# Optimization experiments

Measured on AMD Instinct MI355X. Metric: run time of the kernel, lower is better.

## Reference

```python
import jax, jax.numpy as jnp
import numpy as np
from jax import lax

BN_EPS = 1e-5

# Straight-through-estimator sign (XNOR-Net BinActive): fwd=sign, bwd=clipped identity
@jax.custom_vjp
def ste_sign(x):
    return jnp.sign(x)

def _ste_fwd(x):
    return jnp.sign(x), x

def _ste_bwd(x, g):
    return (g * (jnp.abs(x) <= 1.0).astype(g.dtype),)

ste_sign.defvjp(_ste_fwd, _ste_bwd)

def conv2d(x, w):
    # x: NCHW, w: OIHW, stride 1, VALID
    return lax.conv_general_dilated(x, w, (1, 1), 'VALID',
                                    dimension_numbers=('NCHW', 'OIHW', 'NCHW'))

def maxpool2(x):
    return lax.reduce_window(x, -jnp.inf, lax.max, (1, 1, 2, 2), (1, 1, 2, 2), 'VALID')

def bn2d(x, gamma, beta):
    # training-mode BatchNorm2d: batch stats over (N,H,W), biased variance
    mean = jnp.mean(x, axis=(0, 2, 3), keepdims=True)
    var = jnp.mean((x - mean) ** 2, axis=(0, 2, 3), keepdims=True)
    xhat = (x - mean) * lax.rsqrt(var + BN_EPS)
    return xhat * gamma[None, :, None, None] + beta[None, :, None, None]

def bn1d(x, gamma, beta):
    mean = jnp.mean(x, axis=0, keepdims=True)
    var = jnp.mean((x - mean) ** 2, axis=0, keepdims=True)
    xhat = (x - mean) * lax.rsqrt(var + BN_EPS)
    return xhat * gamma[None, :] + beta[None, :]

def bin_conv2d(x, w):
    # XNOR-style: binarize input and weight, scale by per-filter alpha = mean|W|
    alpha = jnp.mean(jnp.abs(w), axis=(1, 2, 3))  # [O]
    out = conv2d(ste_sign(x), ste_sign(w))
    return out * alpha[None, :, None, None]

def bin_linear(x, w):
    # w: [out_features, in_features]
    alpha = jnp.mean(jnp.abs(w), axis=1)  # [out_features]
    return (ste_sign(x) @ ste_sign(w).T) * alpha[None, :]


def setup_inputs() -> dict:
    key = jax.random.key(0)
    ks = jax.random.split(key, 8)
    B = 8192
    inp = {
        'x': jax.random.normal(ks[0], (B, 1, 28, 28), dtype=jnp.float32),
        'conv1_w': jax.random.normal(ks[1], (20, 1, 5, 5), dtype=jnp.float32) * 0.2,
        'bn1_g': jnp.ones((20,), jnp.float32),
        'bn1_b': jnp.zeros((20,), jnp.float32),
        'conv2_w': jax.random.normal(ks[2], (50, 20, 5, 5), dtype=jnp.float32) * 0.04,
        'bn2_g': jnp.ones((50,), jnp.float32),
        'bn2_b': jnp.zeros((50,), jnp.float32),
        'fc1_w': jax.random.normal(ks[3], (500, 800), dtype=jnp.float32) * 0.035,
        'bn3_g': jnp.ones((500,), jnp.float32),
        'bn3_b': jnp.zeros((500,), jnp.float32),
        'fc2_w': jax.random.normal(ks[4], (10, 500), dtype=jnp.float32) * 0.045,
        'fc2_b': jnp.zeros((10,), jnp.float32),
    }
    return inp


def reference(x, conv1_w, bn1_g, bn1_b, conv2_w, bn2_g, bn2_b,
              fc1_w, bn3_g, bn3_b, fc2_w, fc2_b):
    h = conv2d(x, conv1_w)                 # [B,20,24,24]
    h = jax.nn.relu(bn2d(h, bn1_g, bn1_b))
    h = maxpool2(h)                        # [B,20,12,12]
    h = bin_conv2d(h, conv2_w)             # [B,50,8,8]
    h = jax.nn.relu(bn2d(h, bn2_g, bn2_b))
    h = maxpool2(h)                        # [B,50,4,4]
    h = h.reshape(-1, 50 * 4 * 4)          # [B,800]
    h = bin_linear(h, fc1_w)               # [B,500]
    h = jax.nn.relu(bn1d(h, bn3_g, bn3_b))
    return h @ fc2_w.T + fc2_b[None, :]    # [B,10]
```

## Files before the change

kernel.cpp:

```cpp
#include <hip/hip_runtime.h>
#include <stdint.h>

#define BATCH 8192
#define NJOB  1179648

__global__ __launch_bounds__(256) void k_pack(const float* __restrict__ w2,
    const float* __restrict__ w3, unsigned* __restrict__ wpos2,
    unsigned* __restrict__ wneg2, float* __restrict__ alpha2,
    unsigned* __restrict__ wpos3, unsigned* __restrict__ wneg3,
    float* __restrict__ alpha3, int* __restrict__ flags2, int* __restrict__ flags3){
  __shared__ int zf;
  int tid = threadIdx.x;
  if (tid == 0) zf = 0;
  __syncthreads();
  if (blockIdx.x < 5){
    int t = blockIdx.x*256 + tid;
    int had0 = 0;
    if (t < 1250){
      int o = t/25, k = t%25;
      unsigned p=0, n=0;
      for (int i=0;i<20;i++){
        float v = w2[(o*20+i)*25 + k];
        if (v > 0.f) p |= 1u<<i;
        else if (v < 0.f) n |= 1u<<i;
        else had0 = 1;
      }
      wpos2[t] = p; wneg2[t] = n;
    }
    if (t < 50){
      float s = 0.f;
      for (int i=0;i<500;i++) s += fabsf(w2[t*500+i]);
      alpha2[t] = s / 500.f;
    }
    if (had0) atomicOr(&zf, 1);
    __syncthreads();
    if (tid == 0) flags2[blockIdx.x] = zf;
  } else {
    int t = (blockIdx.x-5)*256 + tid;
    int had0 = 0;
    if (t < 12500){
      int j = t/25, w = t%25;
      unsigned p=0, n=0;
      for (int bb=0;bb<32;bb++){
        float v = w3[j*800 + w*32 + bb];
        if (v > 0.f) p |= 1u<<bb;
        else if (v < 0.f) n |= 1u<<bb;
        else had0 = 1;
      }
      wpos3[t] = p; wneg3[t] = n;
    }
    if (t < 500){
      float s = 0.f;
      for (int i=0;i<800;i++) s += fabsf(w3[t*800+i]);
      alpha3[t] = s / 800.f;
    }
    if (had0) atomicOr(&zf, 1);
    __syncthreads();
    if (tid == 0) flags3[blockIdx.x-5] = zf;
  }
}


#define CONV1_ROWS(IPTR)                                                      \
  float vA0=0.f,vA1=0.f,vA2=0.f,vA3=0.f;                                      \
  float vB0=0.f,vB1=0.f,vB2=0.f,vB3=0.f;                                      \
  _Pragma("unroll")                                                           \
  for (int r=0;r<6;r++){                                                      \
    const float2* rp = (const float2*)((IPTR) + r*28);                        \
    float2 p0 = rp[0], p1 = rp[1], p2 = rp[2];                                \
    float row0=p0.x, row1=p0.y, row2=p1.x, row3=p1.y, row4=p2.x, row5=p2.y;   \
    if (r<5){                                                                 \
      _Pragma("unroll")                                                       \
      for (int kx=0;kx<5;kx++){                                               \
        float e0 = (kx==0?row0:kx==1?row1:kx==2?row2:kx==3?row3:row4);        \
        float e1 = (kx==0?row1:kx==1?row2:kx==2?row3:kx==3?row4:row5);        \
        float w = wa[r*5+kx], u = wb[r*5+kx];                                 \
        vA0=fmaf(e0,w,vA0); vA1=fmaf(e1,w,vA1);                               \
        vB0=fmaf(e0,u,vB0); vB1=fmaf(e1,u,vB1);                               \
      }                                                                       \
    }                                                                         \
    if (r>0){                                                                 \
      _Pragma("unroll")                                                       \
      for (int kx=0;kx<5;kx++){                                               \
        float e0 = (kx==0?row0:kx==1?row1:kx==2?row2:kx==3?row3:row4);        \
        float e1 = (kx==0?row1:kx==1?row2:kx==2?row3:kx==3?row4:row5);        \
        float w = wa[(r-1)*5+kx], u = wb[(r-1)*5+kx];                         \
        vA2=fmaf(e0,w,vA2); vA3=fmaf(e1,w,vA3);                               \
        vB2=fmaf(e0,u,vB2); vB3=fmaf(e1,u,vB3);                               \
      }                                                                       \
    }                                                                         \
  }

template<bool STORE_MM>
__global__ __launch_bounds__(256) void k_conv1_stats(const float* __restrict__ x,
        const float* __restrict__ w1, const float* __restrict__ g1,
        float* __restrict__ part1, float2* __restrict__ c1ext){
  __shared__ float img[8*784];
  __shared__ float wsh[500];
  __shared__ float gsh[20];
  __shared__ float red[4][40];
  int tid = threadIdx.x;
  size_t base = (size_t)blockIdx.x * 8;
  const float4* xv = (const float4*)(x + base*784);
  float4* iv = (float4*)img;
  for (int i=tid;i<1568;i+=256) iv[i] = xv[i];
  for (int i=tid;i<500;i+=256)  wsh[i] = w1[i];
  if (tid < 20) gsh[tid] = g1[tid];
  __syncthreads();
  int lane = tid & 63, wid = tid >> 6;
#pragma unroll 1
  for (int cg=0; cg<10; ++cg){
    float wa[25], wb[25];
#pragma unroll
    for (int k=0;k<25;k++){ wa[k]=wsh[(2*cg)*25+k]; wb[k]=wsh[(2*cg+1)*25+k]; }
    float gA = gsh[2*cg], gB = gsh[2*cg+1];
    float sa=0.f, qa=0.f, sb=0.f, qb=0.f;
#pragma unroll 1
    for (int job=tid; job<8*144; job+=256){
      int li = job/144, pp = job%144;
      int py = pp/12, px = pp%12;
      const float* ip = &img[li*784 + py*56 + px*2];
      CONV1_ROWS(ip)
      sa += (vA0+vA1)+(vA2+vA3);
      qa = fmaf(vA0,vA0, fmaf(vA1,vA1, fmaf(vA2,vA2, fmaf(vA3,vA3, qa))));
      sb += (vB0+vB1)+(vB2+vB3);
      qb = fmaf(vB0,vB0, fmaf(vB1,vB1, fmaf(vB2,vB2, fmaf(vB3,vB3, qb))));
      if (STORE_MM){
        float mxA = fmaxf(fmaxf(vA0,vA1),fmaxf(vA2,vA3));
        float mnA = fminf(fminf(vA0,vA1),fminf(vA2,vA3));
        float mxB = fmaxf(fmaxf(vB0,vB1),fmaxf(vB2,vB3));
        float mnB = fminf(fminf(vB0,vB1),fminf(vB2,vB3));
        float eA = (gA > 0.f) ? mxA : mnA;
        float eB = (gB > 0.f) ? mxB : mnB;
        c1ext[(size_t)cg*NJOB + (base+li)*144 + pp] = make_float2(eA,eB);
      }
    }
#pragma unroll
    for (int d=32; d>0; d>>=1){
      sa += __shfl_down(sa,d); qa += __shfl_down(qa,d);
      sb += __shfl_down(sb,d); qb += __shfl_down(qb,d);
    }
    if (lane==0){
      red[wid][(2*cg)*2]   = sa; red[wid][(2*cg)*2+1]   = qa;
      red[wid][(2*cg+1)*2] = sb; red[wid][(2*cg+1)*2+1] = qb;
    }
  }
  __syncthreads();
  if (tid < 40)
    part1[blockIdx.x*40 + tid] = red[0][tid]+red[1][tid]+red[2][tid]+red[3][tid];
}

__global__ __launch_bounds__(256) void k_reduce1(const float* __restrict__ part1,
        const float* __restrict__ g, const float* __restrict__ b,
        float* __restrict__ s1t1){
  __shared__ double rs[256], rq[256];
  int c = blockIdx.x;
  int tid = threadIdx.x;
  double s=0.0, q=0.0;
  for (int i=tid;i<1024;i+=256){
    s += (double)part1[i*40 + c*2];
    q += (double)part1[i*40 + c*2 + 1];
  }
  rs[tid]=s; rq[tid]=q;
  __syncthreads();
  for (int d=128; d>0; d>>=1){
    if (tid<d){ rs[tid]+=rs[tid+d]; rq[tid]+=rq[tid+d]; }
    __syncthreads();
  }
  if (tid==0){
    double N = 8192.0*576.0;
    double mean = rs[0]/N, var = rq[0]/N - mean*mean;
    double r = 1.0/sqrt(var + 1e-5);
    double sc = (double)g[c]*r;
    s1t1[c*2]   = (float)sc;
    s1t1[c*2+1] = (float)((double)b[c] - mean*sc);
  }
}

__global__ __launch_bounds__(256) void k_conv1_bin(const float* __restrict__ x,
        const float* __restrict__ w1, const float* __restrict__ s1t1,
        unsigned* __restrict__ mask1){
  __shared__ float img[8*784];
  __shared__ float wsh[500];
  __shared__ float st[40];
  __shared__ unsigned lw[8*144];
  int tid = threadIdx.x;
  size_t base = (size_t)blockIdx.x * 8;
  const float4* xv = (const float4*)(x + base*784);
  float4* iv = (float4*)img;
  for (int i=tid;i<1568;i+=256) iv[i] = xv[i];
  for (int i=tid;i<500;i+=256)  wsh[i] = w1[i];
  for (int i=tid;i<8*144;i+=256) lw[i] = 0u;
  if (tid < 40) st[tid] = s1t1[tid];
  __syncthreads();
#pragma unroll 1
  for (int cg=0; cg<10; ++cg){
    float wa[25], wb[25];
#pragma unroll
    for (int k=0;k<25;k++){ wa[k]=wsh[(2*cg)*25+k]; wb[k]=wsh[(2*cg+1)*25+k]; }
    float sA = st[(2*cg)*2],   tA = st[(2*cg)*2+1];
    float sB = st[(2*cg+1)*2], tB = st[(2*cg+1)*2+1];
#pragma unroll 1
    for (int job=tid; job<8*144; job+=256){
      int li = job/144, pp = job%144;
      int py = pp/12, px = pp%12;
      const float* ip = &img[li*784 + py*56 + px*2];
      CONV1_ROWS(ip)
      unsigned bA = (fmaf(vA0,sA,tA) > 0.f) || (fmaf(vA1,sA,tA) > 0.f) ||
                    (fmaf(vA2,sA,tA) > 0.f) || (fmaf(vA3,sA,tA) > 0.f);
      unsigned bB = (fmaf(vB0,sB,tB) > 0.f) || (fmaf(vB1,sB,tB) > 0.f) ||
                    (fmaf(vB2,sB,tB) > 0.f) || (fmaf(vB3,sB,tB) > 0.f);
      lw[job] |= (bA << (2*cg)) | (bB << (2*cg+1));
    }
  }
  __syncthreads();
  for (int i=tid;i<8*144;i+=256){
    int li = i/144, pp = i%144;
    mask1[(base+li)*144 + pp] = lw[i];
  }
}

__global__ __launch_bounds__(256) void k_conv1_bin_lite(const float2* __restrict__ c1ext,
        const float* __restrict__ s1t1, unsigned* __restrict__ mask1){
  __shared__ float st[40];
  int tid = threadIdx.x;
  if (tid < 40) st[tid] = s1t1[tid];
  __syncthreads();
  int J = blockIdx.x*256 + tid;
  unsigned word = 0;
#pragma unroll
  for (int cg=0; cg<10; ++cg){
    float2 v = c1ext[(size_t)cg*NJOB + J];
    float sA = st[4*cg+0], tA = st[4*cg+1];
    float sB = st[4*cg+2], tB = st[4*cg+3];
    word |= ((fmaf(v.x,sA,tA) > 0.f) ? 1u : 0u) << (2*cg);
    word |= ((fmaf(v.y,sB,tB) > 0.f) ? 1u : 0u) << (2*cg+1);
  }
  mask1[J] = word;
}

__global__ __launch_bounds__(256) void k_conv2(const unsigned* __restrict__ mask1,
    const unsigned* __restrict__ wpos, const unsigned* __restrict__ wneg,
    const int* __restrict__ flags2, short* __restrict__ S16){
  __shared__ unsigned m1[4*144];
  __shared__ __align__(16) unsigned wp[1400], wn[1400];
  int tid = threadIdx.x;
  size_t base = (size_t)blockIdx.x * 4;
  bool slow = (flags2[0]|flags2[1]|flags2[2]|flags2[3]|flags2[4]) != 0;
  for (int i=tid;i<4*144;i+=256) m1[i] = mask1[base*144 + i];
  for (int i=tid;i<1400;i+=256){
    int o = i/28, k = i%28;
    wn[i] = (k<25) ? wneg[o*25+k] : 0u;
    if (slow) wp[i] = (k<25) ? wpos[o*25+k] : 0u;
  }
  __syncthreads();
  int lane = tid & 63, wid = tid >> 6;
  int y2 = lane >> 3, x2 = lane & 7;
  unsigned mw[25];
  const unsigned* mrow = &m1[wid*144];
#pragma unroll
  for (int ky=0;ky<5;ky++)
#pragma unroll
    for (int kx=0;kx<5;kx++)
      mw[ky*5+kx] = mrow[(y2+ky)*12 + x2+kx];
  short* sp = &S16[((base+wid)*50)*64 + lane];
  if (!slow){
    int pbase = 0;
#pragma unroll
    for (int k=0;k<25;k++) pbase += __popc(mw[k]);
#pragma unroll 1
    for (int o=0;o<50;o++){
      const uint4* n4 = (const uint4*)&wn[o*28];
      int Sn=0;
#pragma unroll
      for (int g=0; g<6; g++){
        uint4 N = n4[g];
        Sn += __popc(mw[4*g]&N.x) + __popc(mw[4*g+1]&N.y)
            + __popc(mw[4*g+2]&N.z) + __popc(mw[4*g+3]&N.w);
      }
      Sn += __popc(mw[24] & wn[o*28+24]);
      sp[o*64] = (short)(pbase - 2*Sn);
    }
  } else {
#pragma unroll 1
    for (int o=0;o<50;o++){
      const uint4* p4 = (const uint4*)&wp[o*28];
      const uint4* n4 = (const uint4*)&wn[o*28];
      int Sp=0, Sn=0;
#pragma unroll
      for (int g=0; g<6; g++){
        uint4 P = p4[g], N = n4[g];
        Sp += __popc(mw[4*g]&P.x) + __popc(mw[4*g+1]&P.y)
            + __popc(mw[4*g+2]&P.z) + __popc(mw[4*g+3]&P.w);
        Sn += __popc(mw[4*g]&N.x) + __popc(mw[4*g+1]&N.y)
            + __popc(mw[4*g+2]&N.z) + __popc(mw[4*g+3]&N.w);
      }
      Sp += __popc(mw[24] & wp[o*28+24]);
      Sn += __popc(mw[24] & wn[o*28+24]);
      sp[o*64] = (short)(Sp - Sn);
    }
  }
}

__global__ __launch_bounds__(256) void k_stats2(const short* __restrict__ S16,
        int* __restrict__ part2){
  int tid = threadIdx.x;
  int lane = tid & 63, wid = tid >> 6;
  const short* p = S16 + (size_t)blockIdx.x * 32 * 3200;
  int rs[13], rq[13];
#pragma unroll
  for (int k=0;k<13;k++){ rs[k]=0; rq[k]=0; }
#pragma unroll 1
  for (int im=0; im<32; ++im){
    const short* q = p + im*3200 + tid;
#pragma unroll
    for (int k=0;k<13;k++){
      if (wid + 4*k < 50){
        int v = q[256*k];
        rs[k] += v; rq[k] += v*v;
      }
    }
  }
#pragma unroll
  for (int k=0;k<13;k++){
    int o = wid + 4*k;
    if (o < 50){
      int s = rs[k], q2 = rq[k];
#pragma unroll
      for (int d=32; d>0; d>>=1){ s += __shfl_down(s,d); q2 += __shfl_down(q2,d); }
      if (lane==0){
        part2[blockIdx.x*100 + o*2]     = s;
        part2[blockIdx.x*100 + o*2 + 1] = q2;
      }
    }
  }
}

__global__ __launch_bounds__(256) void k_conv2_stats_legacy(const unsigned* __restrict__ mask1,
    const unsigned* __restrict__ wpos, const unsigned* __restrict__ wneg,
    const int* __restrict__ flags2, int* __restrict__ part2){
  __shared__ unsigned m1[4*144];
  __shared__ __align__(16) unsigned wp[1400], wn[1400];
  __shared__ int red[4][100];
  int tid = threadIdx.x;
  size_t base = (size_t)blockIdx.x * 4;
  bool slow = (flags2[0]|flags2[1]|flags2[2]|flags2[3]|flags2[4]) != 0;
  for (int i=tid;i<4*144;i+=256) m1[i] = mask1[base*144 + i];
  for (int i=tid;i<1400;i+=256){
    int o = i/28, k = i%28;
    wn[i] = (k<25) ? wneg[o*25+k] : 0u;
    wp[i] = (k<25) ? wpos[o*25+k] : 0u;
  }
  __syncthreads();
  int lane = tid & 63, wid = tid >> 6;
  int y2 = lane >> 3, x2 = lane & 7;
  unsigned mw[25];
  const unsigned* mrow = &m1[wid*144];
#pragma unroll
  for (int ky=0;ky<5;ky++)
#pragma unroll
    for (int kx=0;kx<5;kx++)
      mw[ky*5+kx] = mrow[(y2+ky)*12 + x2+kx];
#pragma unroll 1
  for (int o=0;o<50;o++){
    const uint4* p4 = (const uint4*)&wp[o*28];
    const uint4* n4 = (const uint4*)&wn[o*28];
    int Sp=0, Sn=0;
#pragma unroll
    for (int g=0; g<6; g++){
      uint4 P = p4[g], N = n4[g];
      Sp += __popc(mw[4*g]&P.x) + __popc(mw[4*g+1]&P.y)
          + __popc(mw[4*g+2]&P.z) + __popc(mw[4*g+3]&P.w);
      Sn += __popc(mw[4*g]&N.x) + __popc(mw[4*g+1]&N.y)
          + __popc(mw[4*g+2]&N.z) + __popc(mw[4*g+3]&N.w);
    }
    Sp += __popc(mw[24] & wp[o*28+24]);
    Sn += __popc(mw[24] & wn[o*28+24]);
    int S = Sp - Sn;
    int rs = S, rq = S*S;
#pragma unroll
    for (int d=32; d>0; d>>=1){ rs += __shfl_down(rs,d); rq += __shfl_down(rq,d); }
    if (lane==0){ red[wid][o*2] = rs; red[wid][o*2+1] = rq; }
  }
  __syncthreads();
  if (tid < 100)
    part2[blockIdx.x*100 + tid] = red[0][tid]+red[1][tid]+red[2][tid]+red[3][tid];
}

__global__ __launch_bounds__(256) void k_reduce2(const int* __restrict__ part2,
        int nchunk, const float* __restrict__ alpha2, const float* __restrict__ g,
        const float* __restrict__ b, float* __restrict__ s2t2){
  __shared__ long long rs[256], rq[256];
  int o = blockIdx.x;
  int tid = threadIdx.x;
  long long s=0, q=0;
  for (int i=tid;i<nchunk;i+=256){
    s += part2[i*100 + o*2];
    q += part2[i*100 + o*2 + 1];
  }
  rs[tid]=s; rq[tid]=q;
  __syncthreads();
  for (int d=128; d>0; d>>=1){
    if (tid<d){ rs[tid]+=rs[tid+d]; rq[tid]+=rq[tid+d]; }
    __syncthreads();
  }
  if (tid==0){
    double N = 8192.0*64.0;
    double meanS = (double)rs[0]/N, E2 = (double)rq[0]/N;
    double varS = E2 - meanS*meanS;
    double a = (double)alpha2[o];
    double mean_g = a*meanS, var_g = a*a*varS;
    double r = 1.0/sqrt(var_g + 1e-5);
    double sc = (double)g[o]*r;
    s2t2[o*2]   = (float)(sc*a);
    s2t2[o*2+1] = (float)((double)b[o] - mean_g*sc);
  }
}

#define BIN2_POOL_BODY                                                        \
    unsigned long long bal = __ballot(cond);                                  \
    unsigned long long t4 = bal | (bal>>1) | (bal>>8) | (bal>>9);             \
    bool pb = (lane < 16) && ((t4 >> (16*(lane>>2) + 2*(lane&3))) & 1ull);    \
    unsigned long long bal2 = __ballot(pb);                                   \
    if (lane==0){                                                             \
      unsigned pooled16 = (unsigned)(bal2 & 0xFFFFull);                       \
      lw[wid*25 + (o>>1)] |= pooled16 << (16*(o&1));                          \
    }

__global__ __launch_bounds__(256) void k_bin2(const unsigned* __restrict__ mask1,
    const unsigned* __restrict__ wpos, const unsigned* __restrict__ wneg,
    const float* __restrict__ s2t2, unsigned* __restrict__ mask2){
  __shared__ unsigned m1[4*144];
  __shared__ __align__(16) unsigned wp[1400], wn[1400];
  __shared__ float st[100];
  __shared__ unsigned lw[100];
  int tid = threadIdx.x;
  size_t base = (size_t)blockIdx.x * 4;
  for (int i=tid;i<4*144;i+=256) m1[i] = mask1[base*144 + i];
  for (int i=tid;i<1400;i+=256){
    int o = i/28, k = i%28;
    wp[i] = (k<25) ? wpos[o*25+k] : 0u;
    wn[i] = (k<25) ? wneg[o*25+k] : 0u;
  }
  if (tid < 100){ st[tid] = s2t2[tid]; lw[tid] = 0u; }
  __syncthreads();
  int lane = tid & 63, wid = tid >> 6;
  int y2 = lane >> 3, x2 = lane & 7;
  unsigned mw[25];
  const unsigned* mrow = &m1[wid*144];
#pragma unroll
  for (int ky=0;ky<5;ky++)
#pragma unroll
    for (int kx=0;kx<5;kx++)
      mw[ky*5+kx] = mrow[(y2+ky)*12 + x2+kx];
#pragma unroll 1
  for (int o=0;o<50;o++){
    const uint4* p4 = (const uint4*)&wp[o*28];
    const uint4* n4 = (const uint4*)&wn[o*28];
    int Sp=0, Sn=0;
#pragma unroll
    for (int g=0; g<6; g++){
      uint4 P = p4[g], N = n4[g];
      Sp += __popc(mw[4*g]&P.x) + __popc(mw[4*g+1]&P.y)
          + __popc(mw[4*g+2]&P.z) + __popc(mw[4*g+3]&P.w);
      Sn += __popc(mw[4*g]&N.x) + __popc(mw[4*g+1]&N.y)
          + __popc(mw[4*g+2]&N.z) + __popc(mw[4*g+3]&N.w);
    }
    Sp += __popc(mw[24] & wp[o*28+24]);
    Sn += __popc(mw[24] & wn[o*28+24]);
    int S = Sp - Sn;
    bool cond = fmaf((float)S, st[o*2], st[o*2+1]) > 0.f;
    BIN2_POOL_BODY
  }
  __syncthreads();
  if (tid < 100) mask2[base*25 + tid] = lw[tid];
}

__global__ __launch_bounds__(256) void k_bin2_lite(const short* __restrict__ S16,
    const float* __restrict__ s2t2, unsigned* __restrict__ mask2){
  __shared__ float st[100];
  __shared__ unsigned lw[100];
  int tid = threadIdx.x;
  if (tid < 100){ st[tid] = s2t2[tid]; lw[tid] = 0u; }
  __syncthreads();
  int lane = tid & 63, wid = tid >> 6;
  size_t img = (size_t)blockIdx.x*4 + wid;
#pragma unroll 1
  for (int o=0;o<50;o++){
    int S = S16[(img*50 + o)*64 + lane];
    bool cond = fmaf((float)S, st[o*2], st[o*2+1]) > 0.f;
    BIN2_POOL_BODY
  }
  __syncthreads();
  if (tid < 100) mask2[blockIdx.x*100 + tid] = lw[tid];
}

__global__ __launch_bounds__(256) void k_fc1(const unsigned* __restrict__ mask2,
    const unsigned* __restrict__ wpos, const unsigned* __restrict__ wneg,
    const int* __restrict__ flags3, short* __restrict__ S3){
  __shared__ unsigned m2s[8*25];
  __shared__ short s3s[8*500];
  int tid = threadIdx.x;
  size_t base = (size_t)blockIdx.x * 8;
  for (int i=tid;i<200;i+=256) m2s[i] = mask2[base*25 + i];
  __syncthreads();
  int f = 0;
  for (int i=0;i<49;i++) f |= flags3[i];
  int bl = tid & 7;
  int jg = tid >> 3;
  const unsigned* mrow = &m2s[bl*25];
  if (f == 0){
    int pbase = 0;
#pragma unroll
    for (int w=0;w<25;w++) pbase += __popc(mrow[w]);
#pragma unroll 1
    for (int j=jg; j<500; j+=32){
      const unsigned* n = &wneg[j*25];
      int Sn = 0;
#pragma unroll
      for (int w=0;w<25;w++) Sn += __popc(mrow[w] & n[w]);
      s3s[bl*500 + j] = (short)(pbase - 2*Sn);
    }
  } else {
#pragma unroll 1
    for (int j=jg; j<500; j+=32){
      const unsigned* p = &wpos[j*25];
      const unsigned* n = &wneg[j*25];
      int S = 0;
#pragma unroll
      for (int w=0;w<25;w++){
        unsigned m = mrow[w];
        S += __popc(m & p[w]) - __popc(m & n[w]);
      }
      s3s[bl*500 + j] = (short)S;
    }
  }
  __syncthreads();
  for (int i=tid;i<8*500;i+=256) S3[base*500 + i] = s3s[i];
}

__global__ __launch_bounds__(256) void k_stats3(const short* __restrict__ S3,
                                                int* __restrict__ part3){
  int tid = threadIdx.x;
  const short* p = &S3[(size_t)blockIdx.x * 64 * 500];
  int s0=0,q0=0,s1=0,q1=0;
  for (int b=0;b<64;b++){
    int v0 = p[b*500 + tid];
    s0 += v0; q0 += v0*v0;
    if (tid < 244){
      int v1 = p[b*500 + tid + 256];
      s1 += v1; q1 += v1*v1;
    }
  }
  part3[blockIdx.x*1000 + tid*2]     = s0;
  part3[blockIdx.x*1000 + tid*2 + 1] = q0;
  if (tid < 244){
    part3[blockIdx.x*1000 + (tid+256)*2]     = s1;
    part3[blockIdx.x*1000 + (tid+256)*2 + 1] = q1;
  }
}

__global__ void k_reduce3(const int* __restrict__ part3, const float* __restrict__ alpha3,
                          const float* __restrict__ g, const float* __restrict__ b,
                          float* __restrict__ s3t3){
  int j = blockIdx.x*256 + threadIdx.x;
  if (j >= 500) return;
  long long s=0, q=0;
  for (int i=0;i<128;i++){
    s += part3[i*1000 + j*2];
    q += part3[i*1000 + j*2 + 1];
  }
  double N = 8192.0;
  double meanS = (double)s/N, E2 = (double)q/N;
  double varS = E2 - meanS*meanS;
  double a = (double)alpha3[j];
  double mean_u = a*meanS, var_u = a*a*varS;
  double r = 1.0/sqrt(var_u + 1e-5);
  double sc = (double)g[j]*r;
  s3t3[j*2]   = (float)(sc*a);
  s3t3[j*2+1] = (float)((double)b[j] - mean_u*sc);
}

__global__ __launch_bounds__(256) void k_final(const short* __restrict__ S3,
    const float* __restrict__ s3t3, const float* __restrict__ fc2w,
    const float* __restrict__ fc2b, float* __restrict__ out){
  __shared__ float w[5000];
  __shared__ float st[1000];
  __shared__ float bias[10];
  int tid = threadIdx.x;
  for (int i=tid;i<5000;i+=256) w[i] = fc2w[i];
  for (int i=tid;i<1000;i+=256) st[i] = s3t3[i];
  if (tid<10) bias[tid] = fc2b[tid];
  __syncthreads();
  int sub = tid & 7;
  int li  = tid >> 3;
  size_t b = (size_t)blockIdx.x*32 + li;
  const short* sp = &S3[b*500];
  float acc[10];
#pragma unroll
  for (int m=0;m<10;m++) acc[m] = 0.f;
#pragma unroll 1
  for (int j=sub; j<500; j+=8){
    float h = fmaf((float)sp[j], st[j*2], st[j*2+1]);
    h = fmaxf(h, 0.f);
#pragma unroll
    for (int m=0;m<10;m++) acc[m] = fmaf(h, w[m*500+j], acc[m]);
  }
#pragma unroll
  for (int m=0;m<10;m++){
    float v = acc[m];
    v += __shfl_xor(v, 1);
    v += __shfl_xor(v, 2);
    v += __shfl_xor(v, 4);
    acc[m] = v;
  }
  if (sub == 0){
#pragma unroll
    for (int m=0;m<10;m++) out[b*10 + m] = acc[m] + bias[m];
  }
}

extern "C" void kernel_launch(void* const* d_in, const int* in_sizes, int n_in,
                              void* d_out, int out_size, void* d_ws, size_t ws_size,
                              hipStream_t stream){
  const float* x    = (const float*)d_in[0];
  const float* w1   = (const float*)d_in[1];
  const float* bn1g = (const float*)d_in[2];
  const float* bn1b = (const float*)d_in[3];
  const float* w2   = (const float*)d_in[4];
  const float* bn2g = (const float*)d_in[5];
  const float* bn2b = (const float*)d_in[6];
  const float* w3   = (const float*)d_in[7];
  const float* bn3g = (const float*)d_in[8];
  const float* bn3b = (const float*)d_in[9];
  const float* w4   = (const float*)d_in[10];
  const float* b4   = (const float*)d_in[11];
  float* out = (float*)d_out;
  (void)in_sizes; (void)n_in; (void)out_size;

  char* wsb = (char*)d_ws;
  size_t off = 0;
  auto alloc = [&](size_t n){ size_t o = off; off = (off + n + 255) & ~(size_t)255; return o; };
  float*    s1t1   = (float*)(wsb + alloc(40*sizeof(float)));
  float*    s2t2   = (float*)(wsb + alloc(100*sizeof(float)));
  float*    s3t3   = (float*)(wsb + alloc(1000*sizeof(float)));
  float*    alpha2 = (float*)(wsb + alloc(50*sizeof(float)));
  float*    alpha3 = (float*)(wsb + alloc(500*sizeof(float)));
  int*      flags2 = (int*)(wsb + alloc(5*4));
  int*      flags3 = (int*)(wsb + alloc(49*4));
  unsigned* wpos2  = (unsigned*)(wsb + alloc(1250*4));
  unsigned* wneg2  = (unsigned*)(wsb + alloc(1250*4));
  unsigned* wpos3  = (unsigned*)(wsb + alloc(12500*4));
  unsigned* wneg3  = (unsigned*)(wsb + alloc(12500*4));
  float*    part1  = (float*)(wsb + alloc(1024*40*4));
  int*      part2  = (int*)(wsb + alloc(2048*100*4));
  int*      part3  = (int*)(wsb + alloc(128*1000*4));
  unsigned* mask1  = (unsigned*)(wsb + alloc((size_t)BATCH*144*4));
  unsigned* mask2  = (unsigned*)(wsb + alloc((size_t)BATCH*25*4));
  short*    S3     = (short*)(wsb + alloc((size_t)BATCH*500*2));
  short*    S16    = (short*)(wsb + alloc((size_t)BATCH*50*64*2));
  bool useS16 = (ws_size >= off);
  float2*   c1ext  = (float2*)(wsb + alloc((size_t)10*NJOB*8));
  bool useMM  = (ws_size >= off);

  hipLaunchKernelGGL(k_pack, dim3(54), dim3(256), 0, stream,
                     w2, w3, wpos2, wneg2, alpha2, wpos3, wneg3, alpha3, flags2, flags3);
  if (useMM)
    hipLaunchKernelGGL(HIP_KERNEL_NAME(k_conv1_stats<true>),  dim3(1024), dim3(256), 0, stream, x, w1, bn1g, part1, c1ext);
  else
    hipLaunchKernelGGL(HIP_KERNEL_NAME(k_conv1_stats<false>), dim3(1024), dim3(256), 0, stream, x, w1, bn1g, part1, c1ext);
  hipLaunchKernelGGL(k_reduce1,      dim3(20),    dim3(256), 0, stream, part1, bn1g, bn1b, s1t1);
  if (useMM)
    hipLaunchKernelGGL(k_conv1_bin_lite, dim3(4608), dim3(256), 0, stream, c1ext, s1t1, mask1);
  else
    hipLaunchKernelGGL(k_conv1_bin,  dim3(1024),  dim3(256), 0, stream, x, w1, s1t1, mask1);
  if (useS16){
    hipLaunchKernelGGL(k_conv2,      dim3(2048),  dim3(256), 0, stream, mask1, wpos2, wneg2, flags2, S16);
    hipLaunchKernelGGL(k_stats2,     dim3(256),   dim3(256), 0, stream, S16, part2);
    hipLaunchKernelGGL(k_reduce2,    dim3(50),    dim3(256), 0, stream, part2, 256, alpha2, bn2g, bn2b, s2t2);
    hipLaunchKernelGGL(k_bin2_lite,  dim3(2048),  dim3(256), 0, stream, S16, s2t2, mask2);
  } else {
    hipLaunchKernelGGL(k_conv2_stats_legacy, dim3(2048), dim3(256), 0, stream, mask1, wpos2, wneg2, flags2, part2);
    hipLaunchKernelGGL(k_reduce2,    dim3(50),    dim3(256), 0, stream, part2, 2048, alpha2, bn2g, bn2b, s2t2);
    hipLaunchKernelGGL(k_bin2,       dim3(2048),  dim3(256), 0, stream, mask1, wpos2, wneg2, s2t2, mask2);
  }
  hipLaunchKernelGGL(k_fc1,          dim3(1024),  dim3(256), 0, stream, mask2, wpos3, wneg3, flags3, S3);
  hipLaunchKernelGGL(k_stats3,       dim3(128),   dim3(256), 0, stream, S3, part3);
  hipLaunchKernelGGL(k_reduce3,      dim3(2),     dim3(256), 0, stream, part3, alpha3, bn3g, bn3b, s3t3);
  hipLaunchKernelGGL(k_final,        dim3(256),   dim3(256), 0, stream, S3, s3t3, w4, b4, out);
}
```

Before: 327.3 us.

## Fuse conv1 binarization into conv2 and BN2-pool into fc1 with stats

```diff
diff --git a/kernel.cpp b/kernel.cpp
--- a/kernel.cpp
+++ b/kernel.cpp
@@ -220,23 +220,81 @@
   }
 }
 
-__global__ __launch_bounds__(256) void k_conv1_bin_lite(const float2* __restrict__ c1ext,
-        const float* __restrict__ s1t1, unsigned* __restrict__ mask1){
+__global__ __launch_bounds__(256) void k_conv2f(const float2* __restrict__ c1ext,
+    const float* __restrict__ s1t1, const unsigned* __restrict__ wpos,
+    const unsigned* __restrict__ wneg, const int* __restrict__ flags2,
+    short* __restrict__ S16){
+  __shared__ unsigned m1[4*144];
   __shared__ float st[40];
-  int tid = threadIdx.x;
+  __shared__ __align__(16) unsigned wp[1400], wn[1400];
+  int tid = threadIdx.x;
+  size_t base = (size_t)blockIdx.x * 4;
+  bool slow = (flags2[0]|flags2[1]|flags2[2]|flags2[3]|flags2[4]) != 0;
   if (tid < 40) st[tid] = s1t1[tid];
-  __syncthreads();
-  int J = blockIdx.x*256 + tid;
-  unsigned word = 0;
-#pragma unroll
-  for (int cg=0; cg<10; ++cg){
-    float2 v = c1ext[(size_t)cg*NJOB + J];
-    float sA = st[4*cg+0], tA = st[4*cg+1];
-    float sB = st[4*cg+2], tB = st[4*cg+3];
-    word |= ((fmaf(v.x,sA,tA) > 0.f) ? 1u : 0u) << (2*cg);
-    word |= ((fmaf(v.y,sB,tB) > 0.f) ? 1u : 0u) << (2*cg+1);
-  }
-  mask1[J] = word;
+  for (int i=tid;i<1400;i+=256){
+    int o = i/28, k = i%28;
+    wn[i] = (k<25) ? wneg[o*25+k] : 0u;
+    if (slow) wp[i] = (k<25) ? wpos[o*25+k] : 0u;
+  }
+  __syncthreads();
+  for (int job=tid; job<4*144; job+=256){
+    int li = job/144, pp = job%144;
+    unsigned word = 0;
+#pragma unroll
+    for (int cg=0; cg<10; ++cg){
+      float2 v = c1ext[(size_t)cg*NJOB + (base+li)*144 + pp];
+      word |= ((fmaf(v.x, st[4*cg+0], st[4*cg+1]) > 0.f) ? 1u : 0u) << (2*cg);
+      word |= ((fmaf(v.y, st[4*cg+2], st[4*cg+3]) > 0.f) ? 1u : 0u) << (2*cg+1);
+    }
+    m1[job] = word;
+  }
+  __syncthreads();
+  int lane = tid & 63, wid = tid >> 6;
+  int y2 = lane >> 3, x2 = lane & 7;
+  unsigned mw[25];
+  const unsigned* mrow = &m1[wid*144];
+#pragma unroll
+  for (int ky=0;ky<5;ky++)
+#pragma unroll
+    for (int kx=0;kx<5;kx++)
+      mw[ky*5+kx] = mrow[(y2+ky)*12 + x2+kx];
+  short* sp = &S16[((base+wid)*50)*64 + lane];
+  if (!slow){
+    int pbase = 0;
+#pragma unroll
+    for (int k=0;k<25;k++) pbase += __popc(mw[k]);
+#pragma unroll 1
+    for (int o=0;o<50;o++){
+      const uint4* n4 = (const uint4*)&wn[o*28];
+      int Sn=0;
+#pragma unroll
+      for (int g=0; g<6; g++){
+        uint4 N = n4[g];
+        Sn += __popc(mw[4*g]&N.x) + __popc(mw[4*g+1]&N.y)
+            + __popc(mw[4*g+2]&N.z) + __popc(mw[4*g+3]&N.w);
+      }
+      Sn += __popc(mw[24] & wn[o*28+24]);
+      sp[o*64] = (short)(pbase - 2*Sn);
+    }
+  } else {
+#pragma unroll 1
+    for (int o=0;o<50;o++){
+      const uint4* p4 = (const uint4*)&wp[o*28];
+      const uint4* n4 = (const uint4*)&wn[o*28];
+      int Sp=0, Sn=0;
+#pragma unroll
+      for (int g=0; g<6; g++){
+        uint4 P = p4[g], N = n4[g];
+        Sp += __popc(mw[4*g]&P.x) + __popc(mw[4*g+1]&P.y)
+            + __popc(mw[4*g+2]&P.z) + __popc(mw[4*g+3]&P.w);
+        Sn += __popc(mw[4*g]&N.x) + __popc(mw[4*g+1]&N.y)
+            + __popc(mw[4*g+2]&N.z) + __popc(mw[4*g+3]&N.w);
+      }
+      Sp += __popc(mw[24] & wp[o*28+24]);
+      Sn += __popc(mw[24] & wn[o*28+24]);
+      sp[o*64] = (short)(Sp - Sn);
+    }
+  }
 }
 
 __global__ __launch_bounds__(256) void k_conv2(const unsigned* __restrict__ mask1,
@@ -334,57 +392,6 @@
       }
     }
   }
-}
-
-__global__ __launch_bounds__(256) void k_conv2_stats_legacy(const unsigned* __restrict__ mask1,
-    const unsigned* __restrict__ wpos, const unsigned* __restrict__ wneg,
-    const int* __restrict__ flags2, int* __restrict__ part2){
-  __shared__ unsigned m1[4*144];
-  __shared__ __align__(16) unsigned wp[1400], wn[1400];
-  __shared__ int red[4][100];
-  int tid = threadIdx.x;
-  size_t base = (size_t)blockIdx.x * 4;
-  bool slow = (flags2[0]|flags2[1]|flags2[2]|flags2[3]|flags2[4]) != 0;
-  for (int i=tid;i<4*144;i+=256) m1[i] = mask1[base*144 + i];
-  for (int i=tid;i<1400;i+=256){
-    int o = i/28, k = i%28;
-    wn[i] = (k<25) ? wneg[o*25+k] : 0u;
-    wp[i] = (k<25) ? wpos[o*25+k] : 0u;
-  }
-  __syncthreads();
-  int lane = tid & 63, wid = tid >> 6;
-  int y2 = lane >> 3, x2 = lane & 7;
-  unsigned mw[25];
-  const unsigned* mrow = &m1[wid*144];
-#pragma unroll
-  for (int ky=0;ky<5;ky++)
-#pragma unroll
-    for (int kx=0;kx<5;kx++)
-      mw[ky*5+kx] = mrow[(y2+ky)*12 + x2+kx];
-#pragma unroll 1
-  for (int o=0;o<50;o++){
-    const uint4* p4 = (const uint4*)&wp[o*28];
-    const uint4* n4 = (const uint4*)&wn[o*28];
-    int Sp=0, Sn=0;
-#pragma unroll
-    for (int g=0; g<6; g++){
-      uint4 P = p4[g], N = n4[g];
-      Sp += __popc(mw[4*g]&P.x) + __popc(mw[4*g+1]&P.y)
-          + __popc(mw[4*g+2]&P.z) + __popc(mw[4*g+3]&P.w);
-      Sn += __popc(mw[4*g]&N.x) + __popc(mw[4*g+1]&N.y)
-          + __popc(mw[4*g+2]&N.z) + __popc(mw[4*g+3]&N.w);
-    }
-    Sp += __popc(mw[24] & wp[o*28+24]);
-    Sn += __popc(mw[24] & wn[o*28+24]);
-    int S = Sp - Sn;
-    int rs = S, rq = S*S;
-#pragma unroll
-    for (int d=32; d>0; d>>=1){ rs += __shfl_down(rs,d); rq += __shfl_down(rq,d); }
-    if (lane==0){ red[wid][o*2] = rs; red[wid][o*2+1] = rq; }
-  }
-  __syncthreads();
-  if (tid < 100)
-    part2[blockIdx.x*100 + tid] = red[0][tid]+red[1][tid]+red[2][tid]+red[3][tid];
 }
 
 __global__ __launch_bounds__(256) void k_reduce2(const int* __restrict__ part2,
@@ -417,6 +424,81 @@
   }
 }
 
+__global__ __launch_bounds__(256) void k_fc1f(const short* __restrict__ S16,
+    const float* __restrict__ s2t2, const unsigned* __restrict__ wpos,
+    const unsigned* __restrict__ wneg, const int* __restrict__ flags3,
+    short* __restrict__ S3, int* __restrict__ part3){
+  __shared__ float st[100];
+  __shared__ unsigned m2s[8*25];
+  __shared__ short s3s[8*500];
+  int tid = threadIdx.x;
+  if (tid < 100) st[tid] = s2t2[tid];
+  if (tid < 200) m2s[tid] = 0u;
+  __syncthreads();
+  int lane = tid & 63, wid = tid >> 6;
+  size_t base = (size_t)blockIdx.x * 8;
+#pragma unroll
+  for (int ii=0; ii<2; ++ii){
+    int img = wid + 4*ii;
+    size_t gimg = base + img;
+#pragma unroll 1
+    for (int o=0;o<50;o++){
+      int S = S16[(gimg*50 + o)*64 + lane];
+      bool cond = fmaf((float)S, st[o*2], st[o*2+1]) > 0.f;
+      unsigned long long bal = __ballot(cond);
+      unsigned long long t4 = bal | (bal>>1) | (bal>>8) | (bal>>9);
+      bool pb = (lane < 16) && ((t4 >> (16*(lane>>2) + 2*(lane&3))) & 1ull);
+      unsigned long long bal2 = __ballot(pb);
+      if (lane==0)
+        m2s[img*25 + (o>>1)] |= ((unsigned)(bal2 & 0xFFFFull)) << (16*(o&1));
+    }
+  }
+  __syncthreads();
+  int f = 0;
+  for (int i=0;i<49;i++) f |= flags3[i];
+  int bl = tid & 7;
+  int jg = tid >> 3;
+  const unsigned* mrow = &m2s[bl*25];
+  if (f == 0){
+    int pbase = 0;
+#pragma unroll
+    for (int w=0;w<25;w++) pbase += __popc(mrow[w]);
+#pragma unroll 1
+    for (int j=jg; j<500; j+=32){
+      const unsigned* n = &wneg[j*25];
+      int Sn = 0;
+#pragma unroll
+      for (int w=0;w<25;w++) Sn += __popc(mrow[w] & n[w]);
+      s3s[bl*500 + j] = (short)(pbase - 2*Sn);
+    }
+  } else {
+#pragma unroll 1
+    for (int j=jg; j<500; j+=32){
+      const unsigned* p = &wpos[j*25];
+      const unsigned* n = &wneg[j*25];
+      int S = 0;
+#pragma unroll
+      for (int w=0;w<25;w++){
+        unsigned m = mrow[w];
+        S += __popc(m & p[w]) - __popc(m & n[w]);
+      }
+      s3s[bl*500 + j] = (short)S;
+    }
+  }
+  __syncthreads();
+  for (int i=tid;i<8*500;i+=256) S3[base*500 + i] = s3s[i];
+  for (int j=tid;j<500;j+=256){
+    int s=0, q=0;
+#pragma unroll
+    for (int im=0;im<8;im++){
+      int v = s3s[im*500 + j];
+      s += v; q += v*v;
+    }
+    part3[blockIdx.x*1000 + j*2]     = s;
+    part3[blockIdx.x*1000 + j*2 + 1] = q;
+  }
+}
+
 #define BIN2_POOL_BODY                                                        \
     unsigned long long bal = __ballot(cond);                                  \
     unsigned long long t4 = bal | (bal>>1) | (bal>>8) | (bal>>9);             \
@@ -427,55 +509,6 @@
       lw[wid*25 + (o>>1)] |= pooled16 << (16*(o&1));                          \
     }
 
-__global__ __launch_bounds__(256) void k_bin2(const unsigned* __restrict__ mask1,
-    const unsigned* __restrict__ wpos, const unsigned* __restrict__ wneg,
-    const float* __restrict__ s2t2, unsigned* __restrict__ mask2){
-  __shared__ unsigned m1[4*144];
-  __shared__ __align__(16) unsigned wp[1400], wn[1400];
-  __shared__ float st[100];
-  __shared__ unsigned lw[100];
-  int tid = threadIdx.x;
-  size_t base = (size_t)blockIdx.x * 4;
-  for (int i=tid;i<4*144;i+=256) m1[i] = mask1[base*144 + i];
-  for (int i=tid;i<1400;i+=256){
-    int o = i/28, k = i%28;
-    wp[i] = (k<25) ? wpos[o*25+k] : 0u;
-    wn[i] = (k<25) ? wneg[o*25+k] : 0u;
-  }
-  if (tid < 100){ st[tid] = s2t2[tid]; lw[tid] = 0u; }
-  __syncthreads();
-  int lane = tid & 63, wid = tid >> 6;
-  int y2 = lane >> 3, x2 = lane & 7;
-  unsigned mw[25];
-  const unsigned* mrow = &m1[wid*144];
-#pragma unroll
-  for (int ky=0;ky<5;ky++)
-#pragma unroll
-    for (int kx=0;kx<5;kx++)
-      mw[ky*5+kx] = mrow[(y2+ky)*12 + x2+kx];
-#pragma unroll 1
-  for (int o=0;o<50;o++){
-    const uint4* p4 = (const uint4*)&wp[o*28];
-    const uint4* n4 = (const uint4*)&wn[o*28];
-    int Sp=0, Sn=0;
-#pragma unroll
-    for (int g=0; g<6; g++){
-      uint4 P = p4[g], N = n4[g];
-      Sp += __popc(mw[4*g]&P.x) + __popc(mw[4*g+1]&P.y)
-          + __popc(mw[4*g+2]&P.z) + __popc(mw[4*g+3]&P.w);
-      Sn += __popc(mw[4*g]&N.x) + __popc(mw[4*g+1]&N.y)
-          + __popc(mw[4*g+2]&N.z) + __popc(mw[4*g+3]&N.w);
-    }
-    Sp += __popc(mw[24] & wp[o*28+24]);
-    Sn += __popc(mw[24] & wn[o*28+24]);
-    int S = Sp - Sn;
-    bool cond = fmaf((float)S, st[o*2], st[o*2+1]) > 0.f;
-    BIN2_POOL_BODY
-  }
-  __syncthreads();
-  if (tid < 100) mask2[base*25 + tid] = lw[tid];
-}
-
 __global__ __launch_bounds__(256) void k_bin2_lite(const short* __restrict__ S16,
     const float* __restrict__ s2t2, unsigned* __restrict__ mask2){
   __shared__ float st[100];
@@ -560,25 +593,34 @@
   }
 }
 
-__global__ void k_reduce3(const int* __restrict__ part3, const float* __restrict__ alpha3,
-                          const float* __restrict__ g, const float* __restrict__ b,
-                          float* __restrict__ s3t3){
-  int j = blockIdx.x*256 + threadIdx.x;
-  if (j >= 500) return;
+__global__ __launch_bounds__(256) void k_reduce3(const int* __restrict__ part3,
+        int nchunk, const float* __restrict__ alpha3, const float* __restrict__ g,
+        const float* __restrict__ b, float* __restrict__ s3t3){
+  __shared__ long long rs[256], rq[256];
+  int j = blockIdx.x;
+  int tid = threadIdx.x;
   long long s=0, q=0;
-  for (int i=0;i<128;i++){
+  for (int i=tid;i<nchunk;i+=256){
     s += part3[i*1000 + j*2];
     q += part3[i*1000 + j*2 + 1];
   }
-  double N = 8192.0;
-  double meanS = (double)s/N, E2 = (double)q/N;
-  double varS = E2 - meanS*meanS;
-  double a = (double)alpha3[j];
-  double mean_u = a*meanS, var_u = a*a*varS;
-  double r = 1.0/sqrt(var_u + 1e-5);
-  double sc = (double)g[j]*r;
-  s3t3[j*2]   = (float)(sc*a);
-  s3t3[j*2+1] = (float)((double)b[j] - mean_u*sc);
+  rs[tid]=s; rq[tid]=q;
+  __syncthreads();
+  for (int d=128; d>0; d>>=1){
+    if (tid<d){ rs[tid]+=rs[tid+d]; rq[tid]+=rq[tid+d]; }
+    __syncthreads();
+  }
+  if (tid==0){
+    double N = 8192.0;
+    double meanS = (double)rs[0]/N, E2 = (double)rq[0]/N;
+    double varS = E2 - meanS*meanS;
+    double a = (double)alpha3[j];
+    double mean_u = a*meanS, var_u = a*a*varS;
+    double r = 1.0/sqrt(var_u + 1e-5);
+    double sc = (double)g[j]*r;
+    s3t3[j*2]   = (float)(sc*a);
+    s3t3[j*2+1] = (float)((double)b[j] - mean_u*sc);
+  }
 }
 
 __global__ __launch_bounds__(256) void k_final(const short* __restrict__ S3,
@@ -654,7 +696,7 @@
   unsigned* wneg3  = (unsigned*)(wsb + alloc(12500*4));
   float*    part1  = (float*)(wsb + alloc(1024*40*4));
   int*      part2  = (int*)(wsb + alloc(2048*100*4));
-  int*      part3  = (int*)(wsb + alloc(128*1000*4));
+  int*      part3  = (int*)(wsb + alloc(1024*1000*4));
   unsigned* mask1  = (unsigned*)(wsb + alloc((size_t)BATCH*144*4));
   unsigned* mask2  = (unsigned*)(wsb + alloc((size_t)BATCH*25*4));
   short*    S3     = (short*)(wsb + alloc((size_t)BATCH*500*2));
@@ -670,22 +712,22 @@
   else
     hipLaunchKernelGGL(HIP_KERNEL_NAME(k_conv1_stats<false>), dim3(1024), dim3(256), 0, stream, x, w1, bn1g, part1, c1ext);
   hipLaunchKernelGGL(k_reduce1,      dim3(20),    dim3(256), 0, stream, part1, bn1g, bn1b, s1t1);
-  if (useMM)
-    hipLaunchKernelGGL(k_conv1_bin_lite, dim3(4608), dim3(256), 0, stream, c1ext, s1t1, mask1);
-  else
+
+  if (useMM && useS16){
+    hipLaunchKernelGGL(k_conv2f,     dim3(2048),  dim3(256), 0, stream, c1ext, s1t1, wpos2, wneg2, flags2, S16);
+    hipLaunchKernelGGL(k_stats2,     dim3(256),   dim3(256), 0, stream, S16, part2);
+    hipLaunchKernelGGL(k_reduce2,    dim3(50),    dim3(256), 0, stream, part2, 256, alpha2, bn2g, bn2b, s2t2);
+    hipLaunchKernelGGL(k_fc1f,       dim3(1024),  dim3(256), 0, stream, S16, s2t2, wpos3, wneg3, flags3, S3, part3);
+    hipLaunchKernelGGL(k_reduce3,    dim3(500),   dim3(256), 0, stream, part3, 1024, alpha3, bn3g, bn3b, s3t3);
+  } else {
     hipLaunchKernelGGL(k_conv1_bin,  dim3(1024),  dim3(256), 0, stream, x, w1, s1t1, mask1);
-  if (useS16){
     hipLaunchKernelGGL(k_conv2,      dim3(2048),  dim3(256), 0, stream, mask1, wpos2, wneg2, flags2, S16);
     hipLaunchKernelGGL(k_stats2,     dim3(256),   dim3(256), 0, stream, S16, part2);
     hipLaunchKernelGGL(k_reduce2,    dim3(50),    dim3(256), 0, stream, part2, 256, alpha2, bn2g, bn2b, s2t2);
     hipLaunchKernelGGL(k_bin2_lite,  dim3(2048),  dim3(256), 0, stream, S16, s2t2, mask2);
-  } else {
-    hipLaunchKernelGGL(k_conv2_stats_legacy, dim3(2048), dim3(256), 0, stream, mask1, wpos2, wneg2, flags2, part2);
-    hipLaunchKernelGGL(k_reduce2,    dim3(50),    dim3(256), 0, stream, part2, 2048, alpha2, bn2g, bn2b, s2t2);
-    hipLaunchKernelGGL(k_bin2,       dim3(2048),  dim3(256), 0, stream, mask1, wpos2, wneg2, s2t2, mask2);
-  }
-  hipLaunchKernelGGL(k_fc1,          dim3(1024),  dim3(256), 0, stream, mask2, wpos3, wneg3, flags3, S3);
-  hipLaunchKernelGGL(k_stats3,       dim3(128),   dim3(256), 0, stream, S3, part3);
-  hipLaunchKernelGGL(k_reduce3,      dim3(2),     dim3(256), 0, stream, part3, alpha3, bn3g, bn3b, s3t3);
+    hipLaunchKernelGGL(k_fc1,        dim3(1024),  dim3(256), 0, stream, mask2, wpos3, wneg3, flags3, S3);
+    hipLaunchKernelGGL(k_stats3,     dim3(128),   dim3(256), 0, stream, S3, part3);
+    hipLaunchKernelGGL(k_reduce3,    dim3(500),   dim3(256), 0, stream, part3, 128, alpha3, bn3g, bn3b, s3t3);
+  }
   hipLaunchKernelGGL(k_final,        dim3(256),   dim3(256), 0, stream, S3, s3t3, w4, b4, out);
 }
```

After: 351.6 us. 7.4% more time.
